# Optimization experiments

Hardware: AMD Instinct MI355X
Metric: run time of the kernel (lower is better)

## Reference

```python
import jax, jax.numpy as jnp
import numpy as np

EMBED = 1024
HEADS = 16
HEAD_DIM = EMBED // HEADS
SCALE = HEAD_DIM ** -0.5


def setup_inputs() -> dict:
    key = jax.random.key(0)
    ks = jax.random.split(key, 11)
    T, B = 2048, 2
    xavier = lambda k: jax.random.uniform(k, (EMBED, EMBED), jnp.float32,
                                          -np.sqrt(6.0 / (2 * EMBED)), np.sqrt(6.0 / (2 * EMBED)))
    return {
        "query": jax.random.normal(ks[0], (T, B, EMBED), jnp.float32),
        "key": jax.random.normal(ks[1], (T, B, EMBED), jnp.float32),
        "value": jax.random.normal(ks[2], (T, B, EMBED), jnp.float32),
        "Wq": xavier(ks[3]), "bq": jnp.zeros((EMBED,), jnp.float32),
        "Wk": xavier(ks[4]), "bk": jnp.zeros((EMBED,), jnp.float32),
        "Wv": xavier(ks[5]), "bv": jnp.zeros((EMBED,), jnp.float32),
        "Wo": xavier(ks[6]), "bo": jnp.zeros((EMBED,), jnp.float32),
    }


def reference(query, key, value, Wq, bq, Wk, bk, Wv, bv, Wo, bo):
    T, B, E = query.shape
    S = key.shape[0]
    # projections (nn.Linear: x @ W.T + b)
    q = (query @ Wq.T + bq) * SCALE
    k = key @ Wk.T + bk
    v = value @ Wv.T + bv
    # [len, B, E] -> [B*H, len, hd]
    def split_heads(x, L):
        return x.reshape(L, B * HEADS, HEAD_DIM).transpose(1, 0, 2)
    q = split_heads(q, T)
    k = split_heads(k, S)
    v = split_heads(v, S)
    # scores [B*H, T, S]
    scores = jnp.einsum('btd,bsd->bts', q, k)
    attn_weights = jax.nn.softmax(scores, axis=-1)
    attn = jnp.einsum('bts,bsd->btd', attn_weights, v)  # [B*H, T, hd]
    attn = attn.transpose(1, 0, 2).reshape(T, B, E)
    out = attn @ Wo.T + bo
    avg_weights = attn_weights.reshape(B, HEADS, T, S).sum(axis=1) / HEADS
    return out, avg_weights
```

## Files before the change

### kernel.cpp

```cpp
#include <hip/hip_runtime.h>
#include <math.h>

#define T_LEN 2048
#define B_SZ 2
#define EMB 1024
#define HEADS 16
#define HD 64
#define BH (B_SZ*HEADS)
#define R_ROWS (T_LEN*B_SZ)

typedef unsigned short u16;
typedef __attribute__((ext_vector_type(8))) short bf16x8;
typedef __attribute__((ext_vector_type(4))) short bf16x4;
typedef __attribute__((ext_vector_type(4))) float f32x4;

#define MFMA32(a,b,c) __builtin_amdgcn_mfma_f32_16x16x32_bf16(a,b,c,0,0,0)
#if __has_builtin(__builtin_amdgcn_mfma_f32_16x16x16_bf16)
#define MFMA16(a,b,c) __builtin_amdgcn_mfma_f32_16x16x16_bf16(a,b,c,0,0,0)
#else
#define MFMA16(a,b,c) __builtin_amdgcn_mfma_f32_16x16x16bf16_1k(a,b,c,0,0,0)
#endif

__device__ __forceinline__ u16 f2bf(float f) {
    union { float f; unsigned int u; } v; v.f = f;
    unsigned int r = v.u + 0x7fffu + ((v.u >> 16) & 1u);
    return (u16)(r >> 16);
}
__device__ __forceinline__ float bf2f(u16 h) {
    union { unsigned int u; float f; } v; v.u = ((unsigned int)h) << 16;
    return v.f;
}
__device__ __forceinline__ ushort4 hi4(float4 x) {
    ushort4 u; u.x = f2bf(x.x); u.y = f2bf(x.y); u.z = f2bf(x.z); u.w = f2bf(x.w); return u;
}
__device__ __forceinline__ ushort4 lo4(float4 x, ushort4 h) {
    ushort4 u;
    u.x = f2bf(x.x - bf2f(h.x));
    u.y = f2bf(x.y - bf2f(h.y));
    u.z = f2bf(x.z - bf2f(h.z));
    u.w = f2bf(x.w - bf2f(h.w));
    return u;
}
__device__ __forceinline__ float exp2f_fast(float x) {
#if __has_builtin(__builtin_amdgcn_exp2f)
    return __builtin_amdgcn_exp2f(x);
#else
    float r; asm("v_exp_f32 %0, %1" : "=v"(r) : "v"(x)); return r;
#endif
}
__device__ __forceinline__ float log2f_fast(float x) {
    float r; asm("v_log_f32 %0, %1" : "=v"(r) : "v"(x)); return r;
}
__device__ __forceinline__ bf16x4 pk_bf16x4(float a, float b, float c, float d) {
    union { unsigned int u[2]; bf16x4 v; } t;
    asm("v_cvt_pk_bf16_f32 %0, %1, %2" : "=v"(t.u[0]) : "v"(a), "v"(b));
    asm("v_cvt_pk_bf16_f32 %0, %1, %2" : "=v"(t.u[1]) : "v"(c), "v"(d));
    return t.v;
}
__device__ __forceinline__ void lds_cp16(u16* lds, const u16* g) {
    __builtin_amdgcn_global_load_lds(
        (const __attribute__((address_space(1))) unsigned int*)(const void*)g,
        (__attribute__((address_space(3))) unsigned int*)(void*)lds,
        16, 0, 0);
}

__global__ __launch_bounds__(256)
void conv3_kernel(const float* __restrict__ s0, const float* __restrict__ s1,
                  const float* __restrict__ s2,
                  u16* __restrict__ h0, u16* __restrict__ h1, u16* __restrict__ h2)
{
    const int g = blockIdx.x >> 11;
    const float* src = (g == 0) ? s0 : (g == 1) ? s1 : s2;
    u16* hi = (g == 0) ? h0 : (g == 1) ? h1 : h2;
    size_t base = ((size_t)(blockIdx.x & 2047)*256 + threadIdx.x)*8;
    float4 a = *(const float4*)(src + base);
    float4 b = *(const float4*)(src + base + 4);
    *(ushort4*)(hi + base)     = hi4(a);
    *(ushort4*)(hi + base + 4) = hi4(b);
}

__global__ __launch_bounds__(256)
void conv4_kernel(const float* __restrict__ s0, const float* __restrict__ s1,
                  const float* __restrict__ s2, const float* __restrict__ s3,
                  u16* __restrict__ h0, u16* __restrict__ l0,
                  u16* __restrict__ h1, u16* __restrict__ l1,
                  u16* __restrict__ h2, u16* __restrict__ l2,
                  u16* __restrict__ h3, u16* __restrict__ l3)
{
    const int g = blockIdx.x >> 9;
    const float* src = (g == 0) ? s0 : (g == 1) ? s1 : (g == 2) ? s2 : s3;
    u16* hi = (g == 0) ? h0 : (g == 1) ? h1 : (g == 2) ? h2 : h3;
    u16* lo = (g == 0) ? l0 : (g == 1) ? l1 : (g == 2) ? l2 : l3;
    size_t base = ((size_t)(blockIdx.x & 511)*256 + threadIdx.x)*8;
    float4 a = *(const float4*)(src + base);
    float4 b = *(const float4*)(src + base + 4);
    ushort4 hh0 = hi4(a), hh1 = hi4(b);
    ushort4 ll0 = lo4(a, hh0), ll1 = lo4(b, hh1);
    *(ushort4*)(hi + base)     = hh0;
    *(ushort4*)(hi + base + 4) = hh1;
    *(ushort4*)(lo + base)     = ll0;
    *(ushort4*)(lo + base + 4) = ll1;
}

__global__ __launch_bounds__(512)
void proj_mfma(const u16* __restrict__ Ahi, const u16* __restrict__ Alo,
               const u16* __restrict__ Bhi, const u16* __restrict__ Blo,
               const float* __restrict__ bias,
               float* __restrict__ outF, u16* __restrict__ outHi, u16* __restrict__ outLo,
               float scale, int mode)
{
    __shared__ __align__(16) u16 sAh[2][128*32];
    __shared__ __align__(16) u16 sAl[2][128*32];
    __shared__ __align__(16) u16 sBh[2][64*32];
    __shared__ __align__(16) u16 sBl[2][64*32];
    const int tid = threadIdx.x;
    const int w = tid >> 6, ln = tid & 63, lm = ln & 15, lq = ln >> 4;
    const int wm = w & 3, wn = w >> 2;
    const int m0 = blockIdx.x * 128, n0 = blockIdx.y * 64;
    const int K = 1024;
    const int ar = ln >> 2;
    const int ac = ln & 3;
    const bool hasAl = (Alo != nullptr);
    const bool hasBl = (Blo != nullptr);

    f32x4 acc[2][2];
#pragma unroll
    for (int i = 0; i < 2; ++i)
#pragma unroll
        for (int j = 0; j < 2; ++j) acc[i][j] = (f32x4){0.f,0.f,0.f,0.f};

    auto stage = [&](int p, int k0) {
        {
            int r = w*16 + ar;
            int c = ac ^ ((r >> 1) & 3);
            size_t g = (size_t)(m0 + r)*K + k0 + c*8;
            lds_cp16(&sAh[p][w*512], Ahi + g);
            if (hasAl) lds_cp16(&sAl[p][w*512], Alo + g);
        }
        {
            int ch = w & 3;
            int r = ch*16 + ar;
            int c = ac ^ ((r >> 1) & 3);
            size_t g = (size_t)(n0 + r)*K + k0 + c*8;
            if (w < 4) lds_cp16(&sBh[p][ch*512], Bhi + g);
            else if (hasBl) lds_cp16(&sBl[p][ch*512], Blo + g);
        }
    };

    stage(0, 0);
    int cur = 0;
    for (int k0 = 0; k0 < 1024; k0 += 32) {
        __syncthreads();
        if (k0 + 32 < 1024) stage(cur ^ 1, k0 + 32);

        bf16x8 afh[2], afl[2], bfh[2], bfl[2];
#pragma unroll
        for (int i = 0; i < 2; ++i) {
            int row = wm*32 + i*16 + lm;
            int off = row*32 + (lq ^ ((row >> 1) & 3))*8;
            afh[i] = *(const bf16x8*)&sAh[cur][off];
            if (hasAl) afl[i] = *(const bf16x8*)&sAl[cur][off];
        }
#pragma unroll
        for (int j = 0; j < 2; ++j) {
            int row = wn*32 + j*16 + lm;
            int off = row*32 + (lq ^ ((row >> 1) & 3))*8;
            bfh[j] = *(const bf16x8*)&sBh[cur][off];
            if (hasBl) bfl[j] = *(const bf16x8*)&sBl[cur][off];
        }
#pragma unroll
        for (int i = 0; i < 2; ++i)
#pragma unroll
            for (int j = 0; j < 2; ++j) {
                f32x4 a = acc[i][j];
                if (hasBl) a = MFMA32(afh[i], bfl[j], a);
                if (hasAl) a = MFMA32(afl[i], bfh[j], a);
                a = MFMA32(afh[i], bfh[j], a);
                acc[i][j] = a;
            }
        cur ^= 1;
    }

    if (mode == 0) {
#pragma unroll
        for (int j = 0; j < 2; ++j) {
            float bv = bias[n0 + wn*32 + j*16 + lm];
#pragma unroll
            for (int i = 0; i < 2; ++i)
#pragma unroll
                for (int r = 0; r < 4; ++r) {
                    int gm = m0 + wm*32 + i*16 + lq*4 + r;
                    outF[(size_t)gm*EMB + n0 + wn*32 + j*16 + lm] = acc[i][j][r] + bv;
                }
        }
    } else if (mode == 1) {
        const int h = n0 >> 6;
#pragma unroll
        for (int j = 0; j < 2; ++j) {
            float bv = bias[n0 + wn*32 + j*16 + lm];
            int d = wn*32 + j*16 + lm;
#pragma unroll
            for (int i = 0; i < 2; ++i)
#pragma unroll
                for (int r = 0; r < 4; ++r) {
                    int gm = m0 + wm*32 + i*16 + lq*4 + r;
                    int t = gm >> 1, bb = gm & 1;
                    float val = (acc[i][j][r] + bv) * scale;
                    u16 hv = f2bf(val);
                    size_t o = ((size_t)(bb*HEADS + h)*T_LEN + t)*HD + d;
                    outHi[o] = hv;
                    if (outLo) outLo[o] = f2bf(val - bf2f(hv));
                }
        }
    } else {
#pragma unroll
        for (int i = 0; i < 2; ++i)
#pragma unroll
            for (int r = 0; r < 4; ++r) {
                int gm = m0 + wm*32 + i*16 + lq*4 + r;
                int h = gm >> 6, d = gm & 63;
                float bv = bias[gm];
#pragma unroll
                for (int j = 0; j < 2; ++j) {
                    int gn = n0 + wn*32 + j*16 + lm;
                    int t = gn >> 1, bb = gn & 1;
                    outHi[((size_t)(bb*HEADS + h)*HD + d)*T_LEN + t] = f2bf(acc[i][j][r] + bv);
                }
            }
    }
}

__global__ __launch_bounds__(256)
void flash_kernel(const u16* __restrict__ qHi,
                  const u16* __restrict__ kHi, const u16* __restrict__ vT,
                  u16* __restrict__ attnHi,
                  float* __restrict__ mbuf, float* __restrict__ lbuf)
{
    __shared__ __align__(16) u16 Khi[2][64*64];
    __shared__ __align__(16) u16 Vts[2][64*64];
    const int tid = threadIdx.x;
    const int w = tid >> 6, ln = tid & 63, lm = ln & 15, lq = ln >> 4;
    const int bh = blockIdx.y;
    const int t0 = blockIdx.x * 64;
    const int b = bh >> 4, hh = bh & 15;
    const int sr = ln >> 3, scc = ln & 7;

    bf16x8 qfhi[2];
    {
        size_t qo = ((size_t)bh*T_LEN + t0 + w*16 + lm)*HD;
#pragma unroll
        for (int f = 0; f < 2; ++f)
            qfhi[f] = *(const bf16x8*)(qHi + qo + f*32 + lq*8);
    }

    f32x4 O[4];
    float m_t = -INFINITY, l_t = 0.f;
#pragma unroll
    for (int dt = 0; dt < 4; ++dt) O[dt] = (f32x4){0.f,0.f,0.f,0.f};

    auto stage = [&](int p, int s0) {
#pragma unroll
        for (int i = 0; i < 2; ++i) {
            int ch = w*2 + i;
            int r = ch*8 + sr;
            int c = scc ^ (r & 7);
            lds_cp16(&Khi[p][ch*512], kHi + ((size_t)bh*T_LEN + s0 + r)*HD + c*8);
            lds_cp16(&Vts[p][ch*512], vT  + ((size_t)bh*HD + r)*T_LEN + s0 + c*8);
        }
    };

    stage(0, 0);
    int cur = 0;
    for (int s0 = 0; s0 < T_LEN; s0 += 64) {
        __syncthreads();
        if (s0 + 64 < T_LEN) stage(cur ^ 1, s0 + 64);

        const u16* __restrict__ KH = Khi[cur];
        const u16* __restrict__ VS = Vts[cur];

        f32x4 S[4];
#pragma unroll
        for (int ms = 0; ms < 4; ++ms) {
            const int kr = ms*16 + lm;
            const int sw = kr & 7;
            const u16* rowH = &KH[kr*64];
            bf16x8 ah0 = *(const bf16x8*)(rowH + ((lq    ) ^ sw)*8);
            bf16x8 ah1 = *(const bf16x8*)(rowH + ((lq + 4) ^ sw)*8);
            __builtin_amdgcn_s_setprio(1);
            f32x4 s4 = {0.f,0.f,0.f,0.f};
            s4 = MFMA32(ah0, qfhi[0], s4);
            s4 = MFMA32(ah1, qfhi[1], s4);
            __builtin_amdgcn_s_setprio(0);
            S[ms] = s4;
        }

        bf16x4 P[4];
        {
            float mx = fmaxf(fmaxf(S[0][0], S[0][1]), fmaxf(S[0][2], S[0][3]));
#pragma unroll
            for (int ms = 1; ms < 4; ++ms)
                mx = fmaxf(mx, fmaxf(fmaxf(S[ms][0], S[ms][1]),
                                     fmaxf(S[ms][2], S[ms][3])));
            mx = fmaxf(mx, __shfl_xor(mx, 16));
            mx = fmaxf(mx, __shfl_xor(mx, 32));
            if (__any(mx > m_t + 8.0f)) {
                float mnew = fmaxf(m_t, mx);
                float alpha = exp2f_fast(m_t - mnew);
                m_t = mnew;
                l_t *= alpha;
                f32x4 av;
#pragma unroll
                for (int r = 0; r < 4; ++r) av[r] = __shfl(alpha, lq*4 + r);
#pragma unroll
                for (int dt = 0; dt < 4; ++dt) O[dt] *= av;
            }
            const float mn = m_t;
            float rs = 0.f;
#pragma unroll
            for (int ms = 0; ms < 4; ++ms) {
                float p0 = exp2f_fast(S[ms][0]-mn);
                float p1 = exp2f_fast(S[ms][1]-mn);
                float p2 = exp2f_fast(S[ms][2]-mn);
                float p3 = exp2f_fast(S[ms][3]-mn);
                rs += (p0+p1)+(p2+p3);
                P[ms] = pk_bf16x4(p0, p1, p2, p3);
            }
            rs += __shfl_xor(rs, 16);
            rs += __shfl_xor(rs, 32);
            l_t += rs;
        }

        __builtin_amdgcn_s_setprio(1);
#pragma unroll
        for (int dt = 0; dt < 4; ++dt) {
            const int d = dt*16 + lm;
            const int dw = d & 7;
#pragma unroll
            for (int ms = 0; ms < 4; ++ms) {
                bf16x4 vf = *(const bf16x4*)&VS[d*64 + ((2*ms + (lq>>1)) ^ dw)*8 + (lq&1)*4];
                O[dt] = MFMA16(P[ms], vf, O[dt]);
            }
        }
        __builtin_amdgcn_s_setprio(0);
        cur ^= 1;
    }

    {
        float inv = 1.0f / l_t;
        f32x4 iv;
#pragma unroll
        for (int r = 0; r < 4; ++r) iv[r] = __shfl(inv, lq*4 + r);
        int tbase = t0 + w*16;
        if (lq == 0) {
            mbuf[(size_t)bh*T_LEN + tbase + lm] = m_t;
            lbuf[(size_t)bh*T_LEN + tbase + lm] = l_t;
        }
#pragma unroll
        for (int dt = 0; dt < 4; ++dt)
#pragma unroll
            for (int r = 0; r < 4; ++r) {
                int t = tbase + lq*4 + r;
                size_t o = ((size_t)t*B_SZ + b)*EMB + hh*HD + dt*16 + lm;
                attnHi[o] = f2bf(O[dt][r] * iv[r]);
            }
    }
}

__global__ __launch_bounds__(512)
void avg_kernel(const u16* __restrict__ qHi,
                const u16* __restrict__ kHi,
                const float* __restrict__ mbuf, const float* __restrict__ lbuf,
                float* __restrict__ avg)
{
    __shared__ __align__(16) u16 Khi[2][128*64];
    const int tid = threadIdx.x;
    const int w = tid >> 6, ln = tid & 63, lm = ln & 15, lq = ln >> 4;
    const int s0 = blockIdx.x * 128;
    const int t0 = blockIdx.y * 128;
    const int b  = blockIdx.z;
    const int sr = ln >> 3, scc = ln & 7;
    f32x4 acc[8];
#pragma unroll
    for (int ms = 0; ms < 8; ++ms) acc[ms] = (f32x4){0.f,0.f,0.f,0.f};

    auto stage = [&](int p, int h) {
        const int bhh = b*HEADS + h;
#pragma unroll
        for (int i = 0; i < 2; ++i) {
            int ch = w*2 + i;
            int r = ch*8 + sr;
            int c = scc ^ (r & 7);
            lds_cp16(&Khi[p][ch*512], kHi + ((size_t)bhh*T_LEN + s0 + r)*HD + c*8);
        }
    };

    stage(0, 0);
    int cur = 0;
    const int t = t0 + w*16 + lm;
    for (int h = 0; h < HEADS; ++h) {
        const int bh = b*HEADS + h;
        bf16x8 qfh[2];
        size_t qo = ((size_t)bh*T_LEN + t)*HD;
#pragma unroll
        for (int f = 0; f < 2; ++f)
            qfh[f] = *(const bf16x8*)(qHi + qo + f*32 + lq*8);
        float mvl = mbuf[(size_t)bh*T_LEN + t]
                  + log2f_fast(lbuf[(size_t)bh*T_LEN + t]) + 4.0f;
        __syncthreads();
        if (h + 1 < HEADS) stage(cur ^ 1, h + 1);

        const u16* __restrict__ KH = Khi[cur];
#pragma unroll
        for (int ms = 0; ms < 8; ++ms) {
            const int kr = ms*16 + lm;
            const int sw = kr & 7;
            const u16* rowH = &KH[kr*64];
            bf16x8 ah0 = *(const bf16x8*)(rowH + ((lq    ) ^ sw)*8);
            bf16x8 ah1 = *(const bf16x8*)(rowH + ((lq + 4) ^ sw)*8);
            f32x4 s4 = {0.f,0.f,0.f,0.f};
            s4 = MFMA32(ah0, qfh[0], s4);
            s4 = MFMA32(ah1, qfh[1], s4);
            f32x4 a = acc[ms];
            a[0] += exp2f_fast(s4[0]-mvl);
            a[1] += exp2f_fast(s4[1]-mvl);
            a[2] += exp2f_fast(s4[2]-mvl);
            a[3] += exp2f_fast(s4[3]-mvl);
            acc[ms] = a;
        }
        cur ^= 1;
    }
#pragma unroll
    for (int ms = 0; ms < 8; ++ms) {
        float4 v;
        v.x = acc[ms][0]; v.y = acc[ms][1];
        v.z = acc[ms][2]; v.w = acc[ms][3];
        *(float4*)(avg + ((size_t)b*T_LEN + t)*T_LEN + s0 + ms*16 + lq*4) = v;
    }
}

extern "C" void kernel_launch(void* const* d_in, const int* in_sizes, int n_in,
                              void* d_out, int out_size, void* d_ws, size_t ws_size,
                              hipStream_t stream)
{
    const float* query = (const float*)d_in[0];
    const float* key   = (const float*)d_in[1];
    const float* value = (const float*)d_in[2];
    const float* Wq = (const float*)d_in[3];
    const float* bq = (const float*)d_in[4];
    const float* Wk = (const float*)d_in[5];
    const float* bk = (const float*)d_in[6];
    const float* Wv = (const float*)d_in[7];
    const float* bv = (const float*)d_in[8];
    const float* Wo = (const float*)d_in[9];
    const float* bo = (const float*)d_in[10];

    float* out = (float*)d_out;
    float* avg = out + (size_t)R_ROWS*EMB;

    const size_t NX = (size_t)R_ROWS*EMB;
    const size_t NW = (size_t)EMB*EMB;
    u16* wsu = (u16*)d_ws;
    u16* cHi  = wsu;            u16* cLo  = cHi + NX;
    u16* WqHi = cLo + NX;       u16* WqLo = WqHi + NW;
    u16* WkHi = WqLo + NW;      u16* WkLo = WkHi + NW;
    u16* WvHi = WkLo + NW;      u16* WvLo = WvHi + NW;
    u16* WoHi = WvLo + NW;      u16* WoLo = WoHi + NW;
    u16* qHi  = WoLo + NW;      u16* xkHi = qHi + NX;
    u16* kHi  = xkHi + NX;      u16* xvHi = kHi + NX;
    u16* vT   = xvHi + NX;
    float* mb = (float*)(vT + NX);
    float* lb = mb + (size_t)BH*T_LEN;

    const float qscale = 0.125f * 1.44269504088896340736f;

    conv4_kernel<<<4*(NW/2048), 256, 0, stream>>>(Wq, Wk, Wv, Wo,
                                                  WqHi, WqLo, WkHi, WkLo,
                                                  WvHi, WvLo, WoHi, WoLo);
    conv3_kernel<<<3*(NX/2048), 256, 0, stream>>>(query, key, value,
                                                  cHi, xkHi, xvHi);

    dim3 gP(R_ROWS/128, EMB/64);
    dim3 gPv(EMB/128, R_ROWS/64);

    proj_mfma<<<gP, 512, 0, stream>>>(cHi,  nullptr, WqHi, WqLo, bq, nullptr, qHi, nullptr, qscale, 1);
    proj_mfma<<<gP, 512, 0, stream>>>(xkHi, nullptr, WkHi, WkLo, bk, nullptr, kHi, nullptr, 1.0f, 1);
    proj_mfma<<<gPv, 512, 0, stream>>>(WvHi, WvLo, xvHi, nullptr, bv, nullptr, vT, nullptr, 1.0f, 2);

    flash_kernel<<<dim3(T_LEN/64, BH), 256, 0, stream>>>(qHi, kHi, vT, cHi, mb, lb);
    proj_mfma<<<gP, 512, 0, stream>>>(cHi, nullptr, WoHi, WoLo, bo, out, nullptr, nullptr, 1.0f, 0);
    avg_kernel<<<dim3(T_LEN/128, T_LEN/128, B_SZ), 512, 0, stream>>>(qHi, kHi, mb, lb, avg);
}
```

Measured before the change: 332.1 us.

## Merge conversion, QKV projection, and output-proj/avg kernels into fewer launches

Fuses the two fp32-to-bf16 conversion kernels into one launch, runs the three Q/K/V projections as one grid indexed by blockIdx.y, and runs the output projection together with the attention-weight averaging kernel in a single launch that shares one LDS buffer. The aim is to cut launch gaps and tail underutilization by letting independent work fill the GPU at the same time. The cost is a larger static LDS footprint for the avg path and branch-based dispatch inside each block. The unused outLo write path is also dropped.

```diff
diff --git a/kernel.cpp b/kernel.cpp
--- a/kernel.cpp
+++ b/kernel.cpp
@@ -65,58 +65,59 @@
 }
 
 __global__ __launch_bounds__(256)
-void conv3_kernel(const float* __restrict__ s0, const float* __restrict__ s1,
-                  const float* __restrict__ s2,
-                  u16* __restrict__ h0, u16* __restrict__ h1, u16* __restrict__ h2)
-{
-    const int g = blockIdx.x >> 11;
-    const float* src = (g == 0) ? s0 : (g == 1) ? s1 : s2;
-    u16* hi = (g == 0) ? h0 : (g == 1) ? h1 : h2;
-    size_t base = ((size_t)(blockIdx.x & 2047)*256 + threadIdx.x)*8;
-    float4 a = *(const float4*)(src + base);
-    float4 b = *(const float4*)(src + base + 4);
-    *(ushort4*)(hi + base)     = hi4(a);
-    *(ushort4*)(hi + base + 4) = hi4(b);
-}
-
-__global__ __launch_bounds__(256)
-void conv4_kernel(const float* __restrict__ s0, const float* __restrict__ s1,
-                  const float* __restrict__ s2, const float* __restrict__ s3,
-                  u16* __restrict__ h0, u16* __restrict__ l0,
-                  u16* __restrict__ h1, u16* __restrict__ l1,
-                  u16* __restrict__ h2, u16* __restrict__ l2,
-                  u16* __restrict__ h3, u16* __restrict__ l3)
-{
-    const int g = blockIdx.x >> 9;
-    const float* src = (g == 0) ? s0 : (g == 1) ? s1 : (g == 2) ? s2 : s3;
-    u16* hi = (g == 0) ? h0 : (g == 1) ? h1 : (g == 2) ? h2 : h3;
-    u16* lo = (g == 0) ? l0 : (g == 1) ? l1 : (g == 2) ? l2 : l3;
-    size_t base = ((size_t)(blockIdx.x & 511)*256 + threadIdx.x)*8;
-    float4 a = *(const float4*)(src + base);
-    float4 b = *(const float4*)(src + base + 4);
-    ushort4 hh0 = hi4(a), hh1 = hi4(b);
-    ushort4 ll0 = lo4(a, hh0), ll1 = lo4(b, hh1);
-    *(ushort4*)(hi + base)     = hh0;
-    *(ushort4*)(hi + base + 4) = hh1;
-    *(ushort4*)(lo + base)     = ll0;
-    *(ushort4*)(lo + base + 4) = ll1;
-}
-
-__global__ __launch_bounds__(512)
-void proj_mfma(const u16* __restrict__ Ahi, const u16* __restrict__ Alo,
+void conv7_kernel(const float* __restrict__ Wq, const float* __restrict__ Wk,
+                  const float* __restrict__ Wv, const float* __restrict__ Wo,
+                  u16* __restrict__ WqHi, u16* __restrict__ WqLo,
+                  u16* __restrict__ WkHi, u16* __restrict__ WkLo,
+                  u16* __restrict__ WvHi, u16* __restrict__ WvLo,
+                  u16* __restrict__ WoHi, u16* __restrict__ WoLo,
+                  const float* __restrict__ xq, const float* __restrict__ xk,
+                  const float* __restrict__ xv,
+                  u16* __restrict__ xqHi, u16* __restrict__ xkHi,
+                  u16* __restrict__ xvHi)
+{
+    if (blockIdx.x < 2048) {
+        const int g = blockIdx.x >> 9;
+        const float* src = (g == 0) ? Wq : (g == 1) ? Wk : (g == 2) ? Wv : Wo;
+        u16* hi = (g == 0) ? WqHi : (g == 1) ? WkHi : (g == 2) ? WvHi : WoHi;
+        u16* lo = (g == 0) ? WqLo : (g == 1) ? WkLo : (g == 2) ? WvLo : WoLo;
+        size_t base = ((size_t)(blockIdx.x & 511)*256 + threadIdx.x)*8;
+        float4 a = *(const float4*)(src + base);
+        float4 b = *(const float4*)(src + base + 4);
+        ushort4 h0 = hi4(a), h1 = hi4(b);
+        *(ushort4*)(hi + base)     = h0;
+        *(ushort4*)(hi + base + 4) = h1;
+        *(ushort4*)(lo + base)     = lo4(a, h0);
+        *(ushort4*)(lo + base + 4) = lo4(b, h1);
+    } else {
+        const int idx = blockIdx.x - 2048;
+        const int g = idx >> 11;
+        const float* src = (g == 0) ? xq : (g == 1) ? xk : xv;
+        u16* hi = (g == 0) ? xqHi : (g == 1) ? xkHi : xvHi;
+        size_t base = ((size_t)(idx & 2047)*256 + threadIdx.x)*8;
+        float4 a = *(const float4*)(src + base);
+        float4 b = *(const float4*)(src + base + 4);
+        *(ushort4*)(hi + base)     = hi4(a);
+        *(ushort4*)(hi + base + 4) = hi4(b);
+    }
+}
+
+__device__ __forceinline__
+void proj_body(u16* __restrict__ smem,
+               const u16* __restrict__ Ahi, const u16* __restrict__ Alo,
                const u16* __restrict__ Bhi, const u16* __restrict__ Blo,
                const float* __restrict__ bias,
-               float* __restrict__ outF, u16* __restrict__ outHi, u16* __restrict__ outLo,
-               float scale, int mode)
-{
-    __shared__ __align__(16) u16 sAh[2][128*32];
-    __shared__ __align__(16) u16 sAl[2][128*32];
-    __shared__ __align__(16) u16 sBh[2][64*32];
-    __shared__ __align__(16) u16 sBl[2][64*32];
+               float* __restrict__ outF, u16* __restrict__ outHi,
+               float scale, int mode, int bxi, int byi)
+{
+    u16* sAh = smem;
+    u16* sAl = smem + 8192;
+    u16* sBh = smem + 16384;
+    u16* sBl = smem + 20480;
     const int tid = threadIdx.x;
     const int w = tid >> 6, ln = tid & 63, lm = ln & 15, lq = ln >> 4;
     const int wm = w & 3, wn = w >> 2;
-    const int m0 = blockIdx.x * 128, n0 = blockIdx.y * 64;
+    const int m0 = bxi * 128, n0 = byi * 64;
     const int K = 1024;
     const int ar = ln >> 2;
     const int ac = ln & 3;
@@ -134,16 +135,16 @@
             int r = w*16 + ar;
             int c = ac ^ ((r >> 1) & 3);
             size_t g = (size_t)(m0 + r)*K + k0 + c*8;
-            lds_cp16(&sAh[p][w*512], Ahi + g);
-            if (hasAl) lds_cp16(&sAl[p][w*512], Alo + g);
+            lds_cp16(sAh + p*4096 + w*512, Ahi + g);
+            if (hasAl) lds_cp16(sAl + p*4096 + w*512, Alo + g);
         }
         {
             int ch = w & 3;
             int r = ch*16 + ar;
             int c = ac ^ ((r >> 1) & 3);
             size_t g = (size_t)(n0 + r)*K + k0 + c*8;
-            if (w < 4) lds_cp16(&sBh[p][ch*512], Bhi + g);
-            else if (hasBl) lds_cp16(&sBl[p][ch*512], Blo + g);
+            if (w < 4) lds_cp16(sBh + p*2048 + ch*512, Bhi + g);
+            else if (hasBl) lds_cp16(sBl + p*2048 + ch*512, Blo + g);
         }
     };
 
@@ -158,15 +159,15 @@
         for (int i = 0; i < 2; ++i) {
             int row = wm*32 + i*16 + lm;
             int off = row*32 + (lq ^ ((row >> 1) & 3))*8;
-            afh[i] = *(const bf16x8*)&sAh[cur][off];
-            if (hasAl) afl[i] = *(const bf16x8*)&sAl[cur][off];
+            afh[i] = *(const bf16x8*)&sAh[cur*4096 + off];
+            if (hasAl) afl[i] = *(const bf16x8*)&sAl[cur*4096 + off];
         }
 #pragma unroll
         for (int j = 0; j < 2; ++j) {
             int row = wn*32 + j*16 + lm;
             int off = row*32 + (lq ^ ((row >> 1) & 3))*8;
-            bfh[j] = *(const bf16x8*)&sBh[cur][off];
-            if (hasBl) bfl[j] = *(const bf16x8*)&sBl[cur][off];
+            bfh[j] = *(const bf16x8*)&sBh[cur*2048 + off];
+            if (hasBl) bfl[j] = *(const bf16x8*)&sBl[cur*2048 + off];
         }
 #pragma unroll
         for (int i = 0; i < 2; ++i)
@@ -206,10 +207,8 @@
                     int gm = m0 + wm*32 + i*16 + lq*4 + r;
                     int t = gm >> 1, bb = gm & 1;
                     float val = (acc[i][j][r] + bv) * scale;
-                    u16 hv = f2bf(val);
                     size_t o = ((size_t)(bb*HEADS + h)*T_LEN + t)*HD + d;
-                    outHi[o] = hv;
-                    if (outLo) outLo[o] = f2bf(val - bf2f(hv));
+                    outHi[o] = f2bf(val);
                 }
         }
     } else {
@@ -228,6 +227,30 @@
                 }
             }
     }
+}
+
+__global__ __launch_bounds__(512)
+void proj_qkv(const u16* __restrict__ xqHi, const u16* __restrict__ xkHi,
+              const u16* __restrict__ xvHi,
+              const u16* __restrict__ WqHi, const u16* __restrict__ WqLo,
+              const u16* __restrict__ WkHi, const u16* __restrict__ WkLo,
+              const u16* __restrict__ WvHi, const u16* __restrict__ WvLo,
+              const float* __restrict__ bq, const float* __restrict__ bk,
+              const float* __restrict__ bv,
+              u16* __restrict__ qHi, u16* __restrict__ kHi, u16* __restrict__ vT,
+              float qscale)
+{
+    __shared__ __align__(16) u16 smem[24576];
+    const int z = blockIdx.y;
+    if (z == 0)
+        proj_body(smem, xqHi, nullptr, WqHi, WqLo, bq, nullptr, qHi,
+                  qscale, 1, blockIdx.x & 31, blockIdx.x >> 5);
+    else if (z == 1)
+        proj_body(smem, xkHi, nullptr, WkHi, WkLo, bk, nullptr, kHi,
+                  1.0f, 1, blockIdx.x & 31, blockIdx.x >> 5);
+    else
+        proj_body(smem, WvHi, WvLo, xvHi, nullptr, bv, nullptr, vT,
+                  1.0f, 2, blockIdx.x & 7, blockIdx.x >> 3);
 }
 
 __global__ __launch_bounds__(256)
@@ -366,18 +389,17 @@
     }
 }
 
-__global__ __launch_bounds__(512)
-void avg_kernel(const u16* __restrict__ qHi,
-                const u16* __restrict__ kHi,
-                const float* __restrict__ mbuf, const float* __restrict__ lbuf,
-                float* __restrict__ avg)
-{
-    __shared__ __align__(16) u16 Khi[2][128*64];
+__device__ __forceinline__
+void avg_body(u16* __restrict__ smem,
+              const u16* __restrict__ qHi, const u16* __restrict__ kHi,
+              const float* __restrict__ mbuf, const float* __restrict__ lbuf,
+              float* __restrict__ avg, int sbx, int tbx, int b)
+{
+    u16* Khi = smem;
     const int tid = threadIdx.x;
     const int w = tid >> 6, ln = tid & 63, lm = ln & 15, lq = ln >> 4;
-    const int s0 = blockIdx.x * 128;
-    const int t0 = blockIdx.y * 128;
-    const int b  = blockIdx.z;
+    const int s0 = sbx * 128;
+    const int t0 = tbx * 128;
     const int sr = ln >> 3, scc = ln & 7;
     f32x4 acc[8];
 #pragma unroll
@@ -390,7 +412,7 @@
             int ch = w*2 + i;
             int r = ch*8 + sr;
             int c = scc ^ (r & 7);
-            lds_cp16(&Khi[p][ch*512], kHi + ((size_t)bhh*T_LEN + s0 + r)*HD + c*8);
+            lds_cp16(Khi + p*8192 + ch*512, kHi + ((size_t)bhh*T_LEN + s0 + r)*HD + c*8);
         }
     };
 
@@ -409,7 +431,7 @@
         __syncthreads();
         if (h + 1 < HEADS) stage(cur ^ 1, h + 1);
 
-        const u16* __restrict__ KH = Khi[cur];
+        const u16* __restrict__ KH = Khi + cur*8192;
 #pragma unroll
         for (int ms = 0; ms < 8; ++ms) {
             const int kr = ms*16 + lm;
@@ -438,6 +460,25 @@
     }
 }
 
+__global__ __launch_bounds__(512)
+void oproj_avg(const u16* __restrict__ attnHi,
+               const u16* __restrict__ WoHi, const u16* __restrict__ WoLo,
+               const float* __restrict__ bo, float* __restrict__ out,
+               const u16* __restrict__ qHi, const u16* __restrict__ kHi,
+               const float* __restrict__ mbuf, const float* __restrict__ lbuf,
+               float* __restrict__ avg)
+{
+    __shared__ __align__(16) u16 smem[24576];
+    if (blockIdx.x < 512) {
+        proj_body(smem, attnHi, nullptr, WoHi, WoLo, bo, out, nullptr,
+                  1.0f, 0, blockIdx.x & 31, blockIdx.x >> 5);
+    } else {
+        const int f = blockIdx.x - 512;
+        avg_body(smem, qHi, kHi, mbuf, lbuf, avg,
+                 f & 15, (f >> 4) & 15, f >> 8);
+    }
+}
+
 extern "C" void kernel_launch(void* const* d_in, const int* in_sizes, int n_in,
                               void* d_out, int out_size, void* d_ws, size_t ws_size,
                               hipStream_t stream)
@@ -473,20 +514,19 @@
 
     const float qscale = 0.125f * 1.44269504088896340736f;
 
-    conv4_kernel<<<4*(NW/2048), 256, 0, stream>>>(Wq, Wk, Wv, Wo,
-                                                  WqHi, WqLo, WkHi, WkLo,
-                                                  WvHi, WvLo, WoHi, WoLo);
-    conv3_kernel<<<3*(NX/2048), 256, 0, stream>>>(query, key, value,
-                                                  cHi, xkHi, xvHi);
-
-    dim3 gP(R_ROWS/128, EMB/64);
-    dim3 gPv(EMB/128, R_ROWS/64);
-
-    proj_mfma<<<gP, 512, 0, stream>>>(cHi,  nullptr, WqHi, WqLo, bq, nullptr, qHi, nullptr, qscale, 1);
-    proj_mfma<<<gP, 512, 0, stream>>>(xkHi, nullptr, WkHi, WkLo, bk, nullptr, kHi, nullptr, 1.0f, 1);
-    proj_mfma<<<gPv, 512, 0, stream>>>(WvHi, WvLo, xvHi, nullptr, bv, nullptr, vT, nullptr, 1.0f, 2);
+    conv7_kernel<<<8192, 256, 0, stream>>>(Wq, Wk, Wv, Wo,
+                                           WqHi, WqLo, WkHi, WkLo,
+                                           WvHi, WvLo, WoHi, WoLo,
+                                           query, key, value,
+                                           cHi, xkHi, xvHi);
+
+    proj_qkv<<<dim3(512, 3), 512, 0, stream>>>(cHi, xkHi, xvHi,
+                                               WqHi, WqLo, WkHi, WkLo, WvHi, WvLo,
+                                               bq, bk, bv,
+                                               qHi, kHi, vT, qscale);
 
     flash_kernel<<<dim3(T_LEN/64, BH), 256, 0, stream>>>(qHi, kHi, vT, cHi, mb, lb);
-    proj_mfma<<<gP, 512, 0, stream>>>(cHi, nullptr, WoHi, WoLo, bo, out, nullptr, nullptr, 1.0f, 0);
-    avg_kernel<<<dim3(T_LEN/128, T_LEN/128, B_SZ), 512, 0, stream>>>(qHi, kHi, mb, lb, avg);
-}
+
+    oproj_avg<<<1024, 512, 0, stream>>>(cHi, WoHi, WoLo, bo, out,
+                                        qHi, kHi, mb, lb, avg);
+}
```

Measured after the change: 323.2 us. 2.7% less time.
